# Optimization experiments

Hardware: AMD Instinct MI355X
Metric: run time of the kernel (lower is better)

Reference implementation:

```python
import jax, jax.numpy as jnp
import numpy as np

D_MODEL = 1024
N_HEADS = 16
HEAD_DIM = D_MODEL // N_HEADS
D_FF = 4096
EPS = 1e-5


def _layer_norm(x, gamma, beta):
    mu = jnp.mean(x, axis=-1, keepdims=True)
    var = jnp.var(x, axis=-1, keepdims=True)
    return (x - mu) * jax.lax.rsqrt(var + EPS) * gamma + beta


def setup_inputs() -> dict:
    key = jax.random.key(0)
    ks = jax.random.split(key, 16)
    B, T, S = 2, 2048, 2048
    s = 1.0 / np.sqrt(D_MODEL)
    inp = {
        "tgt": jax.random.normal(ks[0], (B, T, D_MODEL), jnp.float32),
        "memory": jax.random.normal(ks[1], (B, S, D_MODEL), jnp.float32),
        "wq": jax.random.normal(ks[2], (D_MODEL, D_MODEL), jnp.float32) * s,
        "bq": jnp.zeros((D_MODEL,), jnp.float32),
        "wk": jax.random.normal(ks[3], (D_MODEL, D_MODEL), jnp.float32) * s,
        "bk": jnp.zeros((D_MODEL,), jnp.float32),
        "wv": jax.random.normal(ks[4], (D_MODEL, D_MODEL), jnp.float32) * s,
        "bv": jnp.zeros((D_MODEL,), jnp.float32),
        "wo": jax.random.normal(ks[5], (D_MODEL, D_MODEL), jnp.float32) * s,
        "bo": jnp.zeros((D_MODEL,), jnp.float32),
        "w1": jax.random.normal(ks[6], (D_MODEL, D_FF), jnp.float32) * s,
        "b1": jnp.zeros((D_FF,), jnp.float32),
        "w2": jax.random.normal(ks[7], (D_FF, D_MODEL), jnp.float32) * (1.0 / np.sqrt(D_FF)),
        "b2": jnp.zeros((D_MODEL,), jnp.float32),
        "g1": jnp.ones((D_MODEL,), jnp.float32),
        "be1": jnp.zeros((D_MODEL,), jnp.float32),
        "g2": jnp.ones((D_MODEL,), jnp.float32),
        "be2": jnp.zeros((D_MODEL,), jnp.float32),
    }
    return inp


def reference(tgt, memory, wq, bq, wk, bk, wv, bv, wo, bo, w1, b1, w2, b2, g1, be1, g2, be2):
    B, T, _ = tgt.shape
    S = memory.shape[1]
    scale = HEAD_DIM ** -0.5
    # projections -> [B, H, L, Dh]
    Q = (tgt @ wq + bq).reshape(B, T, N_HEADS, HEAD_DIM).transpose(0, 2, 1, 3)
    K = (memory @ wk + bk).reshape(B, S, N_HEADS, HEAD_DIM).transpose(0, 2, 1, 3)
    V = (memory @ wv + bv).reshape(B, S, N_HEADS, HEAD_DIM).transpose(0, 2, 1, 3)
    scores = jnp.einsum("bhtd,bhsd->bhts", Q, K) * scale
    attn = jax.nn.softmax(scores, axis=-1)  # dropout=0 (eval)
    ctx = jnp.einsum("bhts,bhsd->bhtd", attn, V)
    ctx = ctx.transpose(0, 2, 1, 3).reshape(B, T, D_MODEL)
    attn_out = ctx @ wo + bo
    # post-norm residual blocks
    x = _layer_norm(tgt + attn_out, g1, be1)
    ff = jax.nn.relu(x @ w1 + b1) @ w2 + b2
    out = _layer_norm(x + ff, g2, be2)
    return out
```

## Files before the change

kernel.cpp:

```cpp
#include <hip/hip_runtime.h>


typedef unsigned short u16;
typedef __attribute__((ext_vector_type(8))) short bvec8;
typedef __attribute__((ext_vector_type(4))) float fvec4;
typedef __attribute__((ext_vector_type(4))) unsigned uvec4;

#define MFMA16(a, b, c) __builtin_amdgcn_mfma_f32_16x16x32_bf16((a), (b), (c), 0, 0, 0)

__device__ __forceinline__ u16 f2b(float f) {
  union { float f; unsigned u; } x; x.f = f;
  unsigned u = x.u;
  return (u16)((u + 0x7FFFu + ((u >> 16) & 1u)) >> 16);
}
__device__ __forceinline__ unsigned cvtpk(float lo, float hi) {
  unsigned r;
  asm("v_cvt_pk_bf16_f32 %0, %1, %2" : "=v"(r) : "v"(lo), "v"(hi));
  return r;
}
#define PLSWAP32(a, b) asm("v_permlane32_swap_b32 %0, %1" : "+v"(a), "+v"(b))
#define PLSWAP16(a, b) asm("v_permlane16_swap_b32 %0, %1" : "+v"(a), "+v"(b))

__device__ __forceinline__ void gl_lds16(const u16* g, u16* lds) {
  __builtin_amdgcn_global_load_lds(
      (const __attribute__((address_space(1))) void*)g,
      (__attribute__((address_space(3))) void*)lds, 16, 0, 0);
}

__global__ __launch_bounds__(256) void k_pre(
    const float* __restrict__ tgt, const float* __restrict__ mem,
    const float* __restrict__ wq, const float* __restrict__ wk,
    const float* __restrict__ wv, const float* __restrict__ wo,
    const float* __restrict__ w1, const float* __restrict__ w2,
    u16* __restrict__ tgt_b, u16* __restrict__ mem_b,
    u16* __restrict__ wqT, u16* __restrict__ wkvT, u16* __restrict__ woT,
    u16* __restrict__ w1T, u16* __restrict__ w2T) {
  __shared__ float t[32][33];
  int bb = blockIdx.x;
  if (bb < 8192) {
    const float* in = (bb < 4096) ? tgt : mem;
    u16* outp = (bb < 4096) ? tgt_b : mem_b;
    int i = (bb & 4095) * 256 + threadIdx.x;
    float4 v = ((const float4*)in)[i];
    ushort4 o;
    o.x = f2b(v.x); o.y = f2b(v.y); o.z = f2b(v.z); o.w = f2b(v.w);
    ((ushort4*)outp)[i] = o;
    return;
  }
  int b = bb - 8192;
  const float* W; u16* WT; int K, N, bx, by;
  if (b < 4096) {
    int m = b >> 10, tt = b & 1023;
    bx = tt & 31; by = tt >> 5; K = 1024; N = 1024;
    W = (m == 0) ? wq : (m == 1) ? wk : (m == 2) ? wv : wo;
    WT = (m == 0) ? wqT : (m == 1) ? wkvT : (m == 2) ? wkvT + 1024 * 1024 : woT;
  } else if (b < 8192) {
    int tt = b - 4096; bx = tt & 127; by = tt >> 7; K = 1024; N = 4096;
    W = w1; WT = w1T;
  } else {
    int tt = b - 8192; bx = tt & 31; by = tt >> 5; K = 4096; N = 1024;
    W = w2; WT = w2T;
  }
  int tx = threadIdx.x & 31, ty = threadIdx.x >> 5;
  int n0 = bx * 32, k0 = by * 32;
#pragma unroll
  for (int i = 0; i < 4; i++)
    t[ty + i * 8][tx] = W[(size_t)(k0 + ty + i * 8) * N + n0 + tx];
  __syncthreads();
#pragma unroll
  for (int i = 0; i < 4; i++)
    WT[(size_t)(n0 + ty + i * 8) * K + k0 + tx] = f2b(t[tx][ty + i * 8]);
}

__global__ __launch_bounds__(256, 4) void k_qkv(
    const u16* __restrict__ tgt_b, const u16* __restrict__ mem_b,
    const u16* __restrict__ wqT, const u16* __restrict__ wkvT,
    const float* __restrict__ bq, const float* __restrict__ bk,
    const float* __restrict__ bv,
    u16* __restrict__ Qb, u16* __restrict__ Kb, u16* __restrict__ Vtb) {
  __shared__ u16 S[256 * 64];
  const int tid = threadIdx.x, w = tid >> 6, lane = tid & 63;
  const int q = lane >> 4, l = lane & 15;
  const bool isQ = blockIdx.x < 256;
  const int id = isQ ? blockIdx.x : blockIdx.x - 256;
  const int nx = isQ ? 8 : 16;
  const int m0 = (id / nx) * 128, n0 = (id % nx) * 128;
  const u16* A = isQ ? tgt_b : mem_b;
  const u16* BT = isQ ? wqT : wkvT;
  const int wm = (w >> 1) * 64, wn = (w & 1) * 64;
  const int rowin = lane >> 3, grp = lane & 7;
  const int gcol = ((grp + rowin) & 7) * 8;
  const int kc0 = ((q + 8 - (l & 7)) & 7) * 8;
  const int kc1 = ((q + 12 - (l & 7)) & 7) * 8;
  const u16* gp[8];
  u16* lp[8];
#pragma unroll
  for (int c = 0; c < 8; c++) {
    int r0 = (w * 8 + c) * 8;
    gp[c] = (r0 < 128) ? A + (size_t)(m0 + r0 + rowin) * 1024 + gcol
                       : BT + (size_t)(n0 + r0 - 128 + rowin) * 1024 + gcol;
    lp[c] = &S[r0 * 64];
  }
  fvec4 acc[4][4] = {};
#pragma unroll 1
  for (int k0 = 0; k0 < 1024; k0 += 64) {
#pragma unroll
    for (int c = 0; c < 8; c++) gl_lds16(gp[c] + k0, lp[c]);
    __syncthreads();
#pragma unroll
    for (int kh = 0; kh < 2; kh++) {
      const int kc = kh ? kc1 : kc0;
      bvec8 af[4], bf[4];
#pragma unroll
      for (int i = 0; i < 4; i++) {
        af[i] = *(const bvec8*)&S[(wm + 16 * i + l) * 64 + kc];
        bf[i] = *(const bvec8*)&S[(128 + wn + 16 * i + l) * 64 + kc];
      }
#pragma unroll
      for (int i = 0; i < 4; i++)
#pragma unroll
        for (int j = 0; j < 4; j++)
          acc[i][j] = MFMA16(af[i], bf[j], acc[i][j]);
    }
    __syncthreads();
  }
#pragma unroll
  for (int mi = 0; mi < 4; mi++)
#pragma unroll
    for (int ni = 0; ni < 4; ni++) {
      int row = m0 + wm + mi * 16 + q * 4;
      int col = n0 + wn + ni * 16 + l;
      if (isQ) {
        float bvv = bq[col];
#pragma unroll
        for (int r = 0; r < 4; r++)
          Qb[(size_t)(row + r) * 1024 + col] = f2b((acc[mi][ni][r] + bvv) * 0.125f);
      } else if (col < 1024) {
        float bvv = bk[col];
#pragma unroll
        for (int r = 0; r < 4; r++)
          Kb[(size_t)(row + r) * 1024 + col] = f2b(acc[mi][ni][r] + bvv);
      } else {
        int vcol = col - 1024;
        float bvv = bv[vcol];
        int b = row >> 11, s = row & 2047;
        int h = vcol >> 6, d = vcol & 63;
        ushort4 o;
        o.x = f2b(acc[mi][ni][0] + bvv);
        o.y = f2b(acc[mi][ni][1] + bvv);
        o.z = f2b(acc[mi][ni][2] + bvv);
        o.w = f2b(acc[mi][ni][3] + bvv);
        *(ushort4*)&Vtb[((size_t)(b * 16 + h) * 64 + d) * 2048 + s] = o;
      }
    }
}

template <int TM, int TN>
__global__ __launch_bounds__(256, 4) void k_gemm(
    const u16* __restrict__ A, const u16* __restrict__ BT,
    const float* __restrict__ bias, const float* __restrict__ resid,
    float* __restrict__ outF, u16* __restrict__ outB,
    int M, int N, int Kstride, int Klen, float scale, int flags) {
  constexpr int WM = TM / 2, WN = TN / 2;
  constexpr int MI = WM / 16, NI = WN / 16;
  constexpr int NCALL = (TM + TN) / 32;
  __shared__ u16 S[(TM + TN) * 64];
  const int tid = threadIdx.x, w = tid >> 6, lane = tid & 63;
  const int q = lane >> 4, l = lane & 15;
  const int m0 = blockIdx.y * TM, n0 = blockIdx.x * TN;
  const int kbeg = blockIdx.z * Klen;
  const int wm = (w >> 1) * WM, wn = (w & 1) * WN;
  const int rowin = lane >> 3, grp = lane & 7;
  const int gcol = ((grp + rowin) & 7) * 8;
  const int kc0 = ((q + 8 - (l & 7)) & 7) * 8;
  const int kc1 = ((q + 12 - (l & 7)) & 7) * 8;
  const u16* gp[NCALL];
  u16* lp[NCALL];
#pragma unroll
  for (int c = 0; c < NCALL; c++) {
    int r0 = (w * NCALL + c) * 8;
    gp[c] = (r0 < TM) ? A + (size_t)(m0 + r0 + rowin) * Kstride + kbeg + gcol
                      : BT + (size_t)(n0 + r0 - TM + rowin) * Kstride + kbeg + gcol;
    lp[c] = &S[r0 * 64];
  }
  fvec4 acc[MI][NI] = {};
#pragma unroll 1
  for (int k0 = 0; k0 < Klen; k0 += 64) {
#pragma unroll
    for (int c = 0; c < NCALL; c++) gl_lds16(gp[c] + k0, lp[c]);
    __syncthreads();
#pragma unroll
    for (int kh = 0; kh < 2; kh++) {
      const int kc = kh ? kc1 : kc0;
      bvec8 af[MI], bf[NI];
#pragma unroll
      for (int i = 0; i < MI; i++)
        af[i] = *(const bvec8*)&S[(wm + 16 * i + l) * 64 + kc];
#pragma unroll
      for (int j = 0; j < NI; j++)
        bf[j] = *(const bvec8*)&S[(TM + wn + 16 * j + l) * 64 + kc];
#pragma unroll
      for (int i = 0; i < MI; i++)
#pragma unroll
        for (int j = 0; j < NI; j++)
          acc[i][j] = MFMA16(af[i], bf[j], acc[i][j]);
    }
    __syncthreads();
  }
  if (flags & 16) {
    float* po = outF + (size_t)blockIdx.z * M * N;
#pragma unroll
    for (int mi = 0; mi < MI; mi++)
#pragma unroll
      for (int ni = 0; ni < NI; ni++) {
        int row = m0 + wm + mi * 16 + q * 4;
        int col = n0 + wn + ni * 16 + l;
#pragma unroll
        for (int r = 0; r < 4; r++)
          po[(size_t)(row + r) * N + col] = acc[mi][ni][r];
      }
    return;
  }
#pragma unroll
  for (int mi = 0; mi < MI; mi++)
#pragma unroll
    for (int ni = 0; ni < NI; ni++) {
      int row = m0 + wm + mi * 16 + q * 4;
      int col = n0 + wn + ni * 16 + l;
      float bvv = bias[col];
#pragma unroll
      for (int r = 0; r < 4; r++) {
        float v = (acc[mi][ni][r] + bvv) * scale;
        if (flags & 1) v = fmaxf(v, 0.0f);
        size_t idx = (size_t)(row + r) * N + col;
        if (flags & 8) v += resid[idx];
        if (flags & 2) outB[idx] = f2b(v);
        if (flags & 4) outF[idx] = v;
      }
    }
}

__global__ __launch_bounds__(256, 4) void k_attn(
    const u16* __restrict__ Q, const u16* __restrict__ Kb,
    const u16* __restrict__ Vt, float* __restrict__ opart,
    float* __restrict__ lpart) {
  __shared__ u16 Ks[2][64 * 64];
  __shared__ u16 Vs[2][64 * 64];
  const int tid = threadIdx.x, w = tid >> 6, lane = tid & 63;
  const int q = lane >> 4, l = lane & 15;
  const int bx = blockIdx.x;
  const int blk = (bx & 7) * 64 + (bx >> 3);
  const int bh = blk >> 4, tb = blk & 15;
  const int b = bh >> 4, h = bh & 15;
  const int t0 = tb * 128 + w * 32;
  const int sbeg = blockIdx.y * 1024;
  float* op = opart + (size_t)blockIdx.y * 4096 * 1024;
  float* lp = lpart + (size_t)blockIdx.y * 4096 * 16;
  const u16* Qp = Q + (size_t)(b * 2048 + t0) * 1024 + h * 64;
  const u16* Kp = Kb + (size_t)(b * 2048) * 1024 + h * 64;
  const u16* Vp = Vt + (size_t)bh * 64 * 2048;
  const int rowin = lane >> 3, grp = lane & 7;
  const int gcol = ((grp + rowin) & 7) * 8;
  const int kc0 = ((q + 8 - (l & 7)) & 7) * 8;
  const int kc1 = ((q + 12 - (l & 7)) & 7) * 8;
  bvec8 aQ[2][2];
#pragma unroll
  for (int ti = 0; ti < 2; ti++)
#pragma unroll
    for (int kh = 0; kh < 2; kh++)
      aQ[ti][kh] = *(const bvec8*)&Qp[(size_t)(ti * 16 + l) * 1024 + kh * 32 + q * 8];
  fvec4 o[2][4] = {};
  float ls[2] = {0.f, 0.f};
  auto stage = [&](int bb, int sv) {
    gl_lds16(Kp + (size_t)(sv + w * 8 + rowin) * 1024 + gcol, &Ks[bb][(w * 8) * 64]);
    gl_lds16(Kp + (size_t)(sv + 32 + w * 8 + rowin) * 1024 + gcol, &Ks[bb][(32 + w * 8) * 64]);
    gl_lds16(Vp + (size_t)(w * 8 + rowin) * 2048 + sv + gcol, &Vs[bb][(w * 8) * 64]);
    gl_lds16(Vp + (size_t)(32 + w * 8 + rowin) * 2048 + sv + gcol, &Vs[bb][(32 + w * 8) * 64]);
  };
  stage(0, sbeg);
  int cur = 0;
#pragma unroll 1
  for (int s0 = sbeg; s0 < sbeg + 1024; s0 += 64) {
    __syncthreads();
    if (s0 + 64 < sbeg + 1024) stage(cur ^ 1, s0 + 64);
    const u16* KsC = Ks[cur];
    const u16* VsC = Vs[cur];
    unsigned pw[2][4][2];
#pragma unroll
    for (int ss = 0; ss < 4; ss++) {
      const int ro = (ss * 16 + l) * 64;
      bvec8 kf0 = *(const bvec8*)&KsC[ro + kc0];
      bvec8 kf1 = *(const bvec8*)&KsC[ro + kc1];
#pragma unroll
      for (int ti = 0; ti < 2; ti++) {
        fvec4 sc = {0.f, 0.f, 0.f, 0.f};
        sc = MFMA16(kf0, aQ[ti][0], sc);
        sc = MFMA16(kf1, aQ[ti][1], sc);
        float p0 = __expf(sc[0]), p1 = __expf(sc[1]);
        float p2 = __expf(sc[2]), p3 = __expf(sc[3]);
        ls[ti] += (p0 + p1) + (p2 + p3);
        pw[ti][ss][0] = cvtpk(p0, p1);
        pw[ti][ss][1] = cvtpk(p2, p3);
      }
    }
#pragma unroll
    for (int ti = 0; ti < 2; ti++)
#pragma unroll
      for (int b4 = 0; b4 < 2; b4++)
#pragma unroll
        for (int r2 = 0; r2 < 2; r2++) {
          PLSWAP32(pw[ti][2 * b4][r2], pw[ti][2 * b4 + 1][r2]);
          PLSWAP16(pw[ti][2 * b4][r2], pw[ti][2 * b4 + 1][r2]);
        }
    bvec8 bP[2][2];
#pragma unroll
    for (int ti = 0; ti < 2; ti++)
#pragma unroll
      for (int kh = 0; kh < 2; kh++) {
        uvec4 t = {pw[ti][2 * kh][0], pw[ti][2 * kh][1],
                   pw[ti][2 * kh + 1][0], pw[ti][2 * kh + 1][1]};
        bP[ti][kh] = __builtin_bit_cast(bvec8, t);
      }
#pragma unroll
    for (int dt = 0; dt < 4; dt++) {
      const int ro = (dt * 16 + l) * 64;
      bvec8 v0 = *(const bvec8*)&VsC[ro + kc0];
      bvec8 v1 = *(const bvec8*)&VsC[ro + kc1];
#pragma unroll
      for (int ti = 0; ti < 2; ti++) {
        o[ti][dt] = MFMA16(v0, bP[ti][0], o[ti][dt]);
        o[ti][dt] = MFMA16(v1, bP[ti][1], o[ti][dt]);
      }
    }
    cur ^= 1;
  }
#pragma unroll
  for (int ti = 0; ti < 2; ti++) {
    float s = ls[ti];
    s += __shfl_xor(s, 16, 64);
    s += __shfl_xor(s, 32, 64);
    int trow = b * 2048 + t0 + ti * 16 + l;
    if (q == 0) lp[trow * 16 + h] = s;
#pragma unroll
    for (int dt = 0; dt < 4; dt++)
      *(fvec4*)&op[(size_t)trow * 1024 + h * 64 + dt * 16 + q * 4] = o[ti][dt];
  }
}

__global__ __launch_bounds__(256) void k_actx(const float* __restrict__ opart,
                                              const float* __restrict__ lpart,
                                              u16* __restrict__ ctx) {
  int row = blockIdx.x, c0 = threadIdx.x * 4;
  int h = c0 >> 6;
  float lsum = lpart[row * 16 + h] + lpart[4096 * 16 + row * 16 + h];
  float inv = 1.0f / lsum;
  float4 a = *(const float4*)&opart[(size_t)row * 1024 + c0];
  float4 b = *(const float4*)&opart[(size_t)4096 * 1024 + (size_t)row * 1024 + c0];
  ushort4 o;
  o.x = f2b((a.x + b.x) * inv);
  o.y = f2b((a.y + b.y) * inv);
  o.z = f2b((a.z + b.z) * inv);
  o.w = f2b((a.w + b.w) * inv);
  *(ushort4*)&ctx[(size_t)row * 1024 + c0] = o;
}

__global__ __launch_bounds__(256) void k_lnp(
    const float* __restrict__ parts, int nparts,
    const float* __restrict__ bias, const float* __restrict__ resid,
    const float* __restrict__ g, const float* __restrict__ be,
    float* __restrict__ xf, u16* __restrict__ xb) {
  __shared__ float sm[8];
  int row = blockIdx.x, tid = threadIdx.x;
  size_t base = (size_t)row * 1024;
  const size_t pstride = (size_t)4096 * 1024;
  float v[4], s = 0.f, ss = 0.f;
#pragma unroll
  for (int j = 0; j < 4; j++) {
    int c = tid + j * 256;
    float acc = bias[c] + resid[base + c];
    for (int z = 0; z < nparts; z++) acc += parts[z * pstride + base + c];
    v[j] = acc;
    s += acc; ss += acc * acc;
  }
#pragma unroll
  for (int off = 32; off; off >>= 1) {
    s += __shfl_down(s, off, 64);
    ss += __shfl_down(ss, off, 64);
  }
  int w = tid >> 6;
  if ((tid & 63) == 0) { sm[w] = s; sm[4 + w] = ss; }
  __syncthreads();
  float S = sm[0] + sm[1] + sm[2] + sm[3];
  float SS = sm[4] + sm[5] + sm[6] + sm[7];
  float mean = S * (1.0f / 1024.0f);
  float var = SS * (1.0f / 1024.0f) - mean * mean;
  float rstd = rsqrtf(var + 1e-5f);
#pragma unroll
  for (int j = 0; j < 4; j++) {
    int c = tid + j * 256;
    float o = (v[j] - mean) * rstd * g[c] + be[c];
    xf[base + c] = o;
    if (xb) xb[base + c] = f2b(o);
  }
}

extern "C" void kernel_launch(void* const* d_in, const int* in_sizes, int n_in,
                              void* d_out, int out_size, void* d_ws, size_t ws_size,
                              hipStream_t stream) {
  (void)in_sizes; (void)n_in; (void)out_size; (void)ws_size;
  const float* tgt = (const float*)d_in[0];
  const float* mem = (const float*)d_in[1];
  const float* wq  = (const float*)d_in[2];
  const float* bq  = (const float*)d_in[3];
  const float* wk  = (const float*)d_in[4];
  const float* bk  = (const float*)d_in[5];
  const float* wv  = (const float*)d_in[6];
  const float* bv  = (const float*)d_in[7];
  const float* wo  = (const float*)d_in[8];
  const float* bo  = (const float*)d_in[9];
  const float* w1  = (const float*)d_in[10];
  const float* b1  = (const float*)d_in[11];
  const float* w2  = (const float*)d_in[12];
  const float* b2  = (const float*)d_in[13];
  const float* g1  = (const float*)d_in[14];
  const float* be1 = (const float*)d_in[15];
  const float* g2  = (const float*)d_in[16];
  const float* be2 = (const float*)d_in[17];
  float* out = (float*)d_out;

  char* ws = (char*)d_ws;
  size_t off = 0;
  auto take = [&](size_t bytes) { char* p = ws + off; off += bytes; return p; };
  const size_t MB = 1024 * 1024;
  u16* tgt_b = (u16*)take(8 * MB);
  u16* mem_b = (u16*)take(8 * MB);
  u16* wqT   = (u16*)take(2 * MB);
  u16* wkvT  = (u16*)take(4 * MB);
  u16* woT   = (u16*)take(2 * MB);
  u16* w1T   = (u16*)take(8 * MB);
  u16* w2T   = (u16*)take(8 * MB);
  u16* Qb    = (u16*)take(8 * MB);
  u16* Kb    = (u16*)take(8 * MB);
  u16* Vtb   = (u16*)take(8 * MB);
  u16* ctx   = (u16*)take(8 * MB);
  float* opart = (float*)take(32 * MB);
  float* opj   = (float*)take(32 * MB);
  float* lpart = (float*)take(1 * MB);
  float* xf  = (float*)take(16 * MB);
  u16* xb    = (u16*)take(8 * MB);
  u16* hbuf  = Qb;
  float* fp2 = opart;

  k_pre<<<20480, 256, 0, stream>>>(tgt, mem, wq, wk, wv, wo, w1, w2,
                                   tgt_b, mem_b, wqT, wkvT, woT, w1T, w2T);
  k_qkv<<<768, 256, 0, stream>>>(tgt_b, mem_b, wqT, wkvT, bq, bk, bv,
                                 Qb, Kb, Vtb);
  k_attn<<<dim3(512, 2), 256, 0, stream>>>(Qb, Kb, Vtb, opart, lpart);
  k_actx<<<4096, 256, 0, stream>>>(opart, lpart, ctx);
  k_gemm<64, 128><<<dim3(8, 64, 1), 256, 0, stream>>>(
      ctx, woT, nullptr, nullptr, opj, nullptr,
      4096, 1024, 1024, 1024, 1.0f, 16);
  k_lnp<<<4096, 256, 0, stream>>>(opj, 1, bo, tgt, g1, be1, xf, xb);
  k_gemm<128, 128><<<dim3(32, 32), 256, 0, stream>>>(
      xb, w1T, b1, nullptr, nullptr, hbuf,
      4096, 4096, 1024, 1024, 1.0f, 1 | 2);
  k_gemm<64, 128><<<dim3(8, 64, 2), 256, 0, stream>>>(
      hbuf, w2T, nullptr, nullptr, fp2, nullptr,
      4096, 1024, 4096, 2048, 1.0f, 16);
  k_lnp<<<4096, 256, 0, stream>>>(fp2, 2, b2, xf, g2, be2, out, nullptr);
}
```

Baseline: 384.6 us.

## Load V fragments directly from global into registers and use exp2 softmax

```diff
diff --git a/kernel.cpp b/kernel.cpp
--- a/kernel.cpp
+++ b/kernel.cpp
@@ -12,6 +12,11 @@
   union { float f; unsigned u; } x; x.f = f;
   unsigned u = x.u;
   return (u16)((u + 0x7FFFu + ((u >> 16) & 1u)) >> 16);
+}
+__device__ __forceinline__ float ex2(float x) {
+  float r;
+  asm("v_exp_f32 %0, %1" : "=v"(r) : "v"(x));
+  return r;
 }
 __device__ __forceinline__ unsigned cvtpk(float lo, float hi) {
   unsigned r;
@@ -134,7 +139,8 @@
         float bvv = bq[col];
 #pragma unroll
         for (int r = 0; r < 4; r++)
-          Qb[(size_t)(row + r) * 1024 + col] = f2b((acc[mi][ni][r] + bvv) * 0.125f);
+          Qb[(size_t)(row + r) * 1024 + col] =
+              f2b((acc[mi][ni][r] + bvv) * 0.18033688011112042f);
       } else if (col < 1024) {
         float bvv = bk[col];
 #pragma unroll
@@ -245,7 +251,6 @@
     const u16* __restrict__ Vt, float* __restrict__ opart,
     float* __restrict__ lpart) {
   __shared__ u16 Ks[2][64 * 64];
-  __shared__ u16 Vs[2][64 * 64];
   const int tid = threadIdx.x, w = tid >> 6, lane = tid & 63;
   const int q = lane >> 4, l = lane & 15;
   const int bx = blockIdx.x;
@@ -258,7 +263,7 @@
   float* lp = lpart + (size_t)blockIdx.y * 4096 * 16;
   const u16* Qp = Q + (size_t)(b * 2048 + t0) * 1024 + h * 64;
   const u16* Kp = Kb + (size_t)(b * 2048) * 1024 + h * 64;
-  const u16* Vp = Vt + (size_t)bh * 64 * 2048;
+  const u16* Vl = Vt + (size_t)bh * 64 * 2048 + (size_t)l * 2048 + q * 8;
   const int rowin = lane >> 3, grp = lane & 7;
   const int gcol = ((grp + rowin) & 7) * 8;
   const int kc0 = ((q + 8 - (l & 7)) & 7) * 8;
@@ -271,20 +276,23 @@
       aQ[ti][kh] = *(const bvec8*)&Qp[(size_t)(ti * 16 + l) * 1024 + kh * 32 + q * 8];
   fvec4 o[2][4] = {};
   float ls[2] = {0.f, 0.f};
-  auto stage = [&](int bb, int sv) {
+  auto stageK = [&](int bb, int sv) {
     gl_lds16(Kp + (size_t)(sv + w * 8 + rowin) * 1024 + gcol, &Ks[bb][(w * 8) * 64]);
     gl_lds16(Kp + (size_t)(sv + 32 + w * 8 + rowin) * 1024 + gcol, &Ks[bb][(32 + w * 8) * 64]);
-    gl_lds16(Vp + (size_t)(w * 8 + rowin) * 2048 + sv + gcol, &Vs[bb][(w * 8) * 64]);
-    gl_lds16(Vp + (size_t)(32 + w * 8 + rowin) * 2048 + sv + gcol, &Vs[bb][(32 + w * 8) * 64]);
   };
-  stage(0, sbeg);
+  stageK(0, sbeg);
   int cur = 0;
 #pragma unroll 1
   for (int s0 = sbeg; s0 < sbeg + 1024; s0 += 64) {
     __syncthreads();
-    if (s0 + 64 < sbeg + 1024) stage(cur ^ 1, s0 + 64);
+    bvec8 vf[4][2];
+#pragma unroll
+    for (int dt = 0; dt < 4; dt++)
+#pragma unroll
+      for (int kh = 0; kh < 2; kh++)
+        vf[dt][kh] = *(const bvec8*)&Vl[(size_t)dt * 16 * 2048 + s0 + kh * 32];
+    if (s0 + 64 < sbeg + 1024) stageK(cur ^ 1, s0 + 64);
     const u16* KsC = Ks[cur];
-    const u16* VsC = Vs[cur];
     unsigned pw[2][4][2];
 #pragma unroll
     for (int ss = 0; ss < 4; ss++) {
@@ -296,8 +304,8 @@
         fvec4 sc = {0.f, 0.f, 0.f, 0.f};
         sc = MFMA16(kf0, aQ[ti][0], sc);
         sc = MFMA16(kf1, aQ[ti][1], sc);
-        float p0 = __expf(sc[0]), p1 = __expf(sc[1]);
-        float p2 = __expf(sc[2]), p3 = __expf(sc[3]);
+        float p0 = ex2(sc[0]), p1 = ex2(sc[1]);
+        float p2 = ex2(sc[2]), p3 = ex2(sc[3]);
         ls[ti] += (p0 + p1) + (p2 + p3);
         pw[ti][ss][0] = cvtpk(p0, p1);
         pw[ti][ss][1] = cvtpk(p2, p3);
@@ -322,16 +330,12 @@
         bP[ti][kh] = __builtin_bit_cast(bvec8, t);
       }
 #pragma unroll
-    for (int dt = 0; dt < 4; dt++) {
-      const int ro = (dt * 16 + l) * 64;
-      bvec8 v0 = *(const bvec8*)&VsC[ro + kc0];
-      bvec8 v1 = *(const bvec8*)&VsC[ro + kc1];
+    for (int dt = 0; dt < 4; dt++)
 #pragma unroll
       for (int ti = 0; ti < 2; ti++) {
-        o[ti][dt] = MFMA16(v0, bP[ti][0], o[ti][dt]);
-        o[ti][dt] = MFMA16(v1, bP[ti][1], o[ti][dt]);
-      }
-    }
+        o[ti][dt] = MFMA16(vf[dt][0], bP[ti][0], o[ti][dt]);
+        o[ti][dt] = MFMA16(vf[dt][1], bP[ti][1], o[ti][dt]);
+      }
     cur ^= 1;
   }
 #pragma unroll
```

New measurement: 429.0 us. 11.5% more time.
